# Optimization experiments

Measured on AMD Instinct MI355X. Metric: run time of the kernel, lower is better.

The kernel has to match this reference:

```python
import jax, jax.numpy as jnp
import numpy as np

BH, L, D = 32, 2048, 64  # (batch*heads), seq_len, d_k

def setup_inputs() -> dict:
    key = jax.random.key(0)
    kq, kk, kv = jax.random.split(key, 3)
    q = jax.random.normal(kq, (BH, L, D), dtype=jnp.float32)
    k = jax.random.normal(kk, (BH, L, D), dtype=jnp.float32)
    v = jax.random.normal(kv, (BH, L, D), dtype=jnp.float32)
    # causal mask: True = masked (future positions), broadcast to all heads
    causal = jnp.triu(jnp.ones((L, L), dtype=jnp.bool_), k=1)
    mask = jnp.broadcast_to(causal, (BH, L, L))
    return {"q": q, "k": k, "v": v, "mask": mask}

def reference(q, k, v, mask):
    # attn = softmax(q @ k^T / sqrt(d_k)) with masked positions set to -inf;
    # dropout is identity in eval mode.
    scale = 1.0 / np.sqrt(D).astype(np.float32)
    scores = jnp.einsum('bld,bmd->blm', q, k) * scale  # (BH, L, L)
    scores = jnp.where(mask, -jnp.inf, scores)
    p = jax.nn.softmax(scores, axis=-1)
    return jnp.einsum('blm,bmd->bld', p, v)  # (BH, L, D)
```

## Files before the change

kernel.cpp:

```cpp
#include <hip/hip_runtime.h>
#include <hip/hip_bf16.h>


#define LEN 2048
#define DD  64
#define BQ  128
#define BK  64
#define NQT 16
#define NKT 32
#define TSHORTS 9216
#define TBYTES  18432

typedef short s16x8 __attribute__((ext_vector_type(8)));
typedef float f32x4 __attribute__((ext_vector_type(4)));
typedef int   i32x2 __attribute__((ext_vector_type(2)));

__device__ __forceinline__ short bfbits(float f) {
  union { float f; unsigned u; } a; a.f = f;
  unsigned u = a.u;
  u += 0x7fffu + ((u >> 16) & 1u);
  return (short)(u >> 16);
}

#define SCL (0.125f * 1.44269504088896f)

__global__ __launch_bounds__(256, 4)
void prep(const float* __restrict__ K, const float* __restrict__ V,
          short* __restrict__ KVp)
{
  const int b = blockIdx.x, t = threadIdx.x;
  if (b < 2048) {
    const int u = b * 256 + t;
    const int chunk = u & 7;
    const int row = (u >> 3) & 63;
    const int ht  = u >> 9;
    const float* src = K + ((size_t)ht * 64 + row) * 64 + chunk * 8;
    const float4 a = *(const float4*)src;
    const float4 c = *(const float4*)(src + 4);
    s16x8 o;
    o[0] = bfbits(a.x); o[1] = bfbits(a.y); o[2] = bfbits(a.z); o[3] = bfbits(a.w);
    o[4] = bfbits(c.x); o[5] = bfbits(c.y); o[6] = bfbits(c.z); o[7] = bfbits(c.w);
    *(s16x8*)(KVp + (size_t)ht * TSHORTS + row * 72 + chunk * 8) = o;
  } else {
    const int u = (b - 2048) * 256 + t;
    const int d = u & 63;
    const int chunk = (u >> 6) & 7;
    const int ht = u >> 9;
    const float* src = V + (size_t)ht * 4096 + (size_t)chunk * 8 * 64 + d;
    s16x8 o;
    #pragma unroll
    for (int j = 0; j < 8; ++j) o[j] = bfbits(src[j * 64]);
    *(s16x8*)(KVp + (size_t)ht * TSHORTS + 4608 + d * 72 + chunk * 8) = o;
  }
}

__device__ __forceinline__ void ld16(const void* g, void* l) {
  __builtin_amdgcn_global_load_lds(
      (const __attribute__((address_space(1))) unsigned int*)g,
      (__attribute__((address_space(3))) unsigned int*)l, 16, 0, 0);
}

__device__ __forceinline__ void stage18k(const char* g, char* l,
                                         int wave, int lane) {
  const int o0 = wave * 1024 + lane * 16;
  ld16(g + o0,          l + o0);
  ld16(g + o0 + 4096,   l + o0 + 4096);
  ld16(g + o0 + 8192,   l + o0 + 8192);
  ld16(g + o0 + 12288,  l + o0 + 12288);
  if (wave < 2) ld16(g + o0 + 16384, l + o0 + 16384);
}

__device__ __forceinline__ int cvtpk(float lo, float hi) {
  int r;
  asm("v_cvt_pk_bf16_f32 %0, %1, %2" : "=v"(r) : "v"(lo), "v"(hi));
  return r;
}

__global__ __launch_bounds__(256, 2)
void fattn(const short* __restrict__ KVp, const float* __restrict__ Qg,
           float* __restrict__ Og)
{
  __shared__ __align__(16) short kv2[2][TSHORTS];
  __shared__ __align__(16) short pb[4][2][16][72];

  const int bx = blockIdx.x;
  const int bh = bx & 31;
  const int grp = bx >> 5;
  const int qt = (grp < 8) ? (15 - grp) : (grp - 8);
  const int q0 = qt * BQ;
  const int tid = threadIdx.x;
  const int wave = tid >> 6, lane = tid & 63;
  const int lq = lane & 15, quad = lane >> 4;
  const int rowb0 = q0 + wave * 32;

  const char* gtiles = (const char*)(KVp + (size_t)bh * NKT * TSHORTS);
  const int ntiles = 2 * qt + 2;

  stage18k(gtiles, (char*)kv2[0], wave, lane);

  s16x8 qf[2][2];
  #pragma unroll
  for (int rb = 0; rb < 2; ++rb) {
    const float* qrow = Qg + ((size_t)bh * LEN + rowb0 + rb * 16 + lq) * DD;
    #pragma unroll
    for (int c = 0; c < 2; ++c) {
      const float4 a = *(const float4*)(qrow + c * 32 + quad * 8);
      const float4 b = *(const float4*)(qrow + c * 32 + quad * 8 + 4);
      s16x8 t;
      t[0] = bfbits(a.x * SCL); t[1] = bfbits(a.y * SCL);
      t[2] = bfbits(a.z * SCL); t[3] = bfbits(a.w * SCL);
      t[4] = bfbits(b.x * SCL); t[5] = bfbits(b.y * SCL);
      t[6] = bfbits(b.z * SCL); t[7] = bfbits(b.w * SCL);
      qf[rb][c] = t;
    }
  }

  f32x4 o[2][4];
  float l[2] = {0.f, 0.f};
  #pragma unroll
  for (int rb = 0; rb < 2; ++rb)
    #pragma unroll
    for (int nt = 0; nt < 4; ++nt) o[rb][nt] = (f32x4){0.f, 0.f, 0.f, 0.f};

  for (int it = 0; it < ntiles; ++it) {
    __syncthreads();
    if (it + 1 < ntiles)
      stage18k(gtiles + (size_t)(it + 1) * TBYTES,
               (char*)kv2[(it + 1) & 1], wave, lane);

    const int k0 = it * BK;
    if (k0 > rowb0 + 31) continue;
    const short* kb = kv2[it & 1];

    f32x4 s0[4], s1[4];
    __builtin_amdgcn_s_setprio(1);
    #pragma unroll
    for (int nt = 0; nt < 4; ++nt) {
      f32x4 a0 = (f32x4){0.f, 0.f, 0.f, 0.f};
      f32x4 a1 = (f32x4){0.f, 0.f, 0.f, 0.f};
      #pragma unroll
      for (int c = 0; c < 2; ++c) {
        const s16x8 kf = *(const s16x8*)&kb[(nt * 16 + lq) * 72 + c * 32 + quad * 8];
        a0 = __builtin_amdgcn_mfma_f32_16x16x32_bf16(kf, qf[0][c], a0, 0, 0, 0);
        a1 = __builtin_amdgcn_mfma_f32_16x16x32_bf16(kf, qf[1][c], a1, 0, 0, 0);
      }
      s0[nt] = a0; s1[nt] = a1;
    }
    __builtin_amdgcn_s_setprio(0);

    auto smpack = [&](f32x4 (&s)[4], const int rowb, float& lacc, int rb) {
      if (k0 + BK - 1 > rowb) {
        #pragma unroll
        for (int nt = 0; nt < 4; ++nt)
          #pragma unroll
          for (int r = 0; r < 4; ++r)
            if (k0 + nt * 16 + quad * 4 + r > rowb + lq) s[nt][r] = -1e30f;
      }
      #pragma unroll
      for (int nt = 0; nt < 4; ++nt)
        #pragma unroll
        for (int r = 0; r < 4; ++r)
          s[nt][r] = __builtin_amdgcn_exp2f(s[nt][r]);
      float t = 0.f;
      #pragma unroll
      for (int nt = 0; nt < 4; ++nt)
        t += (s[nt][0] + s[nt][1]) + (s[nt][2] + s[nt][3]);
      lacc += t;
      #pragma unroll
      for (int nt = 0; nt < 4; ++nt) {
        i32x2 w;
        w[0] = cvtpk(s[nt][0], s[nt][1]);
        w[1] = cvtpk(s[nt][2], s[nt][3]);
        *(i32x2*)&pb[wave][rb][lq][nt * 16 + quad * 4] = w;
      }
    };
    smpack(s0, rowb0,      l[0], 0);
    smpack(s1, rowb0 + 16, l[1], 1);

    const s16x8 pf00 = *(const s16x8*)&pb[wave][0][lq][quad * 8];
    const s16x8 pf01 = *(const s16x8*)&pb[wave][0][lq][32 + quad * 8];
    const s16x8 pf10 = *(const s16x8*)&pb[wave][1][lq][quad * 8];
    const s16x8 pf11 = *(const s16x8*)&pb[wave][1][lq][32 + quad * 8];

    __builtin_amdgcn_s_setprio(1);
    #pragma unroll
    for (int nt = 0; nt < 4; ++nt) {
      const s16x8 vf0 = *(const s16x8*)&kb[4608 + (nt * 16 + lq) * 72 + quad * 8];
      const s16x8 vf1 = *(const s16x8*)&kb[4608 + (nt * 16 + lq) * 72 + 32 + quad * 8];
      o[0][nt] = __builtin_amdgcn_mfma_f32_16x16x32_bf16(pf00, vf0, o[0][nt], 0, 0, 0);
      o[0][nt] = __builtin_amdgcn_mfma_f32_16x16x32_bf16(pf01, vf1, o[0][nt], 0, 0, 0);
      o[1][nt] = __builtin_amdgcn_mfma_f32_16x16x32_bf16(pf10, vf0, o[1][nt], 0, 0, 0);
      o[1][nt] = __builtin_amdgcn_mfma_f32_16x16x32_bf16(pf11, vf1, o[1][nt], 0, 0, 0);
    }
    __builtin_amdgcn_s_setprio(0);
  }

  #pragma unroll
  for (int rb = 0; rb < 2; ++rb) {
    float rs = l[rb];
    rs += __shfl_xor(rs, 16, 64);
    rs += __shfl_xor(rs, 32, 64);
    #pragma unroll
    for (int r = 0; r < 4; ++r) {
      const float inv = 1.0f / __shfl(rs, quad * 4 + r, 64);
      float* orow = Og + ((size_t)bh * LEN + rowb0 + rb * 16 + quad * 4 + r) * DD;
      #pragma unroll
      for (int nt = 0; nt < 4; ++nt)
        orow[nt * 16 + lq] = o[rb][nt][r] * inv;
    }
  }
}

extern "C" void kernel_launch(void* const* d_in, const int* in_sizes, int n_in,
                              void* d_out, int out_size, void* d_ws, size_t ws_size,
                              hipStream_t stream) {
  (void)in_sizes; (void)n_in; (void)out_size; (void)ws_size;
  const float* q = (const float*)d_in[0];
  const float* k = (const float*)d_in[1];
  const float* v = (const float*)d_in[2];
  float* out = (float*)d_out;

  short* KVp = (short*)d_ws;

  prep<<<dim3(4096), dim3(256), 0, stream>>>(k, v, KVp);
  fattn<<<dim3(32 * NQT), dim3(256), 0, stream>>>(KVp, q, out);
}
```

Before: 641.8 us.

## Triple-buffer KV tiles with prefetch distance two and explicit vmcnt waits

Moves from double to triple buffering of K/V tiles in LDS, prefetching two tiles ahead. A hand-written s_waitcnt vmcnt plus a raw s_barrier waits only for the older tile's loads instead of draining everything. Staging is redistributed so each wave issues exactly five loads, and Q global loads are hoisted ahead of the KV staging. LDS use rises by about 18KB per block, which may reduce occupancy at 2 blocks/CU, and the fixed vmcnt count depends on each wave having exactly five outstanding loads.

```diff
diff --git a/kernel.cpp b/kernel.cpp
--- a/kernel.cpp
+++ b/kernel.cpp
@@ -60,14 +60,16 @@
       (__attribute__((address_space(3))) unsigned int*)l, 16, 0, 0);
 }
 
-__device__ __forceinline__ void stage18k(const char* g, char* l,
-                                         int wave, int lane) {
-  const int o0 = wave * 1024 + lane * 16;
-  ld16(g + o0,          l + o0);
-  ld16(g + o0 + 4096,   l + o0 + 4096);
-  ld16(g + o0 + 8192,   l + o0 + 8192);
-  ld16(g + o0 + 12288,  l + o0 + 12288);
-  if (wave < 2) ld16(g + o0 + 16384, l + o0 + 16384);
+__device__ __forceinline__ void stage5(const char* g, char* l,
+                                       int wave, int lane) {
+  const char* gw = g + wave * 4608;
+  char*       lw = l + wave * 4608;
+  const int o = lane * 16;
+  ld16(gw + o,        lw + o);
+  ld16(gw + 1024 + o, lw + 1024 + o);
+  ld16(gw + 2048 + o, lw + 2048 + o);
+  ld16(gw + 3072 + o, lw + 3072 + o);
+  ld16(gw + 3584 + o, lw + 3584 + o);
 }
 
 __device__ __forceinline__ int cvtpk(float lo, float hi) {
@@ -80,7 +82,7 @@
 void fattn(const short* __restrict__ KVp, const float* __restrict__ Qg,
            float* __restrict__ Og)
 {
-  __shared__ __align__(16) short kv2[2][TSHORTS];
+  __shared__ __align__(16) short kv3[3][TSHORTS];
   __shared__ __align__(16) short pb[4][2][16][72];
 
   const int bx = blockIdx.x;
@@ -96,16 +98,27 @@
   const char* gtiles = (const char*)(KVp + (size_t)bh * NKT * TSHORTS);
   const int ntiles = 2 * qt + 2;
 
-  stage18k(gtiles, (char*)kv2[0], wave, lane);
-
-  s16x8 qf[2][2];
+  float4 qraw[2][2][2];
   #pragma unroll
   for (int rb = 0; rb < 2; ++rb) {
     const float* qrow = Qg + ((size_t)bh * LEN + rowb0 + rb * 16 + lq) * DD;
     #pragma unroll
     for (int c = 0; c < 2; ++c) {
-      const float4 a = *(const float4*)(qrow + c * 32 + quad * 8);
-      const float4 b = *(const float4*)(qrow + c * 32 + quad * 8 + 4);
+      qraw[rb][c][0] = *(const float4*)(qrow + c * 32 + quad * 8);
+      qraw[rb][c][1] = *(const float4*)(qrow + c * 32 + quad * 8 + 4);
+    }
+  }
+
+  stage5(gtiles,          (char*)kv3[0], wave, lane);
+  stage5(gtiles + TBYTES, (char*)kv3[1], wave, lane);
+
+  s16x8 qf[2][2];
+  #pragma unroll
+  for (int rb = 0; rb < 2; ++rb)
+    #pragma unroll
+    for (int c = 0; c < 2; ++c) {
+      const float4 a = qraw[rb][c][0];
+      const float4 b = qraw[rb][c][1];
       s16x8 t;
       t[0] = bfbits(a.x * SCL); t[1] = bfbits(a.y * SCL);
       t[2] = bfbits(a.z * SCL); t[3] = bfbits(a.w * SCL);
@@ -113,7 +126,6 @@
       t[6] = bfbits(b.z * SCL); t[7] = bfbits(b.w * SCL);
       qf[rb][c] = t;
     }
-  }
 
   f32x4 o[2][4];
   float l[2] = {0.f, 0.f};
@@ -123,14 +135,22 @@
     for (int nt = 0; nt < 4; ++nt) o[rb][nt] = (f32x4){0.f, 0.f, 0.f, 0.f};
 
   for (int it = 0; it < ntiles; ++it) {
-    __syncthreads();
-    if (it + 1 < ntiles)
-      stage18k(gtiles + (size_t)(it + 1) * TBYTES,
-               (char*)kv2[(it + 1) & 1], wave, lane);
+    __builtin_amdgcn_sched_barrier(0);
+    if (it + 1 < ntiles) {
+      asm volatile("s_waitcnt vmcnt(5)" ::: "memory");
+    } else {
+      asm volatile("s_waitcnt vmcnt(0)" ::: "memory");
+    }
+    __builtin_amdgcn_s_barrier();
+    __builtin_amdgcn_sched_barrier(0);
+
+    if (it + 2 < ntiles)
+      stage5(gtiles + (size_t)(it + 2) * TBYTES,
+             (char*)kv3[(it + 2) % 3], wave, lane);
 
     const int k0 = it * BK;
     if (k0 > rowb0 + 31) continue;
-    const short* kb = kv2[it & 1];
+    const short* kb = kv3[it % 3];
 
     f32x4 s0[4], s1[4];
     __builtin_amdgcn_s_setprio(1);
```

Result: no change. 644.6 us (+0.4%).
